# Optimization experiments

Hardware: AMD Instinct MI355X
Metric: run time of the kernel (lower is better)

Reference implementation:

```python
import jax, jax.numpy as jnp
import numpy as np

HIDDEN = 256


def setup_inputs() -> dict:
    key = jax.random.key(0)
    ks = jax.random.split(key, 6)
    b, c_len, q_len, h = 32, 1024, 128, HIDDEN
    # Xavier-uniform bounds for the learned weights
    lim_vec = float(np.sqrt(6.0 / (h + 1)))      # (h, 1) weights
    lim_cq = float(np.sqrt(6.0 / (1 + h)))       # (1, 1, h) weight
    return {
        "context": jax.random.normal(ks[0], (b, c_len, h), dtype=jnp.float32),
        "query": jax.random.normal(ks[1], (b, q_len, h), dtype=jnp.float32),
        "c_mask": jnp.zeros((b, c_len), dtype=bool),
        "q_mask": jnp.zeros((b, q_len), dtype=bool),
        "c_weight": jax.random.uniform(ks[2], (h, 1), jnp.float32, -lim_vec, lim_vec),
        "q_weight": jax.random.uniform(ks[3], (h, 1), jnp.float32, -lim_vec, lim_vec),
        "cq_weight": jax.random.uniform(ks[4], (1, 1, h), jnp.float32, -lim_cq, lim_cq),
        "bias": jnp.zeros((1,), dtype=jnp.float32),
    }


def reference(context, query, c_mask, q_mask, c_weight, q_weight, cq_weight, bias):
    # Trilinear similarity: S[b,i,j] = c_i.w_c + q_j.w_q + (c_i * w_cq).q_j + bias
    s0 = context @ c_weight                                  # (b, c, 1)
    s1 = jnp.swapaxes(query @ q_weight, 1, 2)                # (b, 1, q)
    s2 = jnp.einsum('bch,bqh->bcq', context * cq_weight, query)
    S = s0 + s1 + s2 + bias                                  # (b, c, q)

    S_bar = jax.nn.softmax(S, axis=1)       # softmax over context axis
    S_bar_bar = jax.nn.softmax(S, axis=2)   # softmax over query axis

    A = jnp.einsum('bcq,bqh->bch', S, query)  # note: raw S, as in source
    B = jnp.einsum('bcq,bkq,bkh->bch', S_bar, S_bar_bar, context)

    return jnp.concatenate([context, A, context * A, context * B], axis=2)
```

## Files before the change

kernel.cpp:

```cpp
#include <hip/hip_runtime.h>
#include <cstdint>
#include <cstddef>

#define BATCH 32
#define CLEN  1024
#define QLEN  128
#define HID   256

typedef __attribute__((ext_vector_type(8))) short bf16x8;
typedef __attribute__((ext_vector_type(4))) float f32x4;

#define MFMA(a, b, c) __builtin_amdgcn_mfma_f32_16x16x32_bf16((a), (b), (c), 0, 0, 0)

__device__ __forceinline__ ushort f2b(float f) {
    union { float f; uint u; } v; v.f = f;
    uint r = (v.u + 0x7fffu + ((v.u >> 16) & 1u)) >> 16;
    return (ushort)r;
}
__device__ __forceinline__ float b2f(ushort u) {
    union { uint u; float f; } v; v.u = ((uint)u) << 16;
    return v.f;
}

__global__ __launch_bounds__(256) void prep_kernel(
    const float* __restrict__ context, const float* __restrict__ query,
    const float* __restrict__ cw, const float* __restrict__ qw,
    const float* __restrict__ cqw,
    ushort* __restrict__ ctxB, ushort* __restrict__ ctxT,
    ushort* __restrict__ qmB, ushort* __restrict__ qT,
    float* __restrict__ cdot, float* __restrict__ qdot)
{
    __shared__ ushort lds[64][258];
    int bid = blockIdx.x;
    int t = threadIdx.x;
    int r = t >> 2, qd = t & 3;
    if (bid < 512) {
        int b = bid >> 4, c0 = (bid & 15) * 64;
        const float* src = context + ((size_t)(b * CLEN + c0 + r)) * HID;
        ushort* cbr = ctxB + ((size_t)(b * CLEN + c0 + r)) * HID;
        float dot = 0.f;
        #pragma unroll
        for (int j = 0; j < 16; j++) {
            int h = j * 16 + qd * 4;
            float4 v = *reinterpret_cast<const float4*>(src + h);
            float4 w = *reinterpret_cast<const float4*>(cw + h);
            dot += v.x * w.x + v.y * w.y + v.z * w.z + v.w * w.w;
            uint p0 = (uint)f2b(v.x) | ((uint)f2b(v.y) << 16);
            uint p1 = (uint)f2b(v.z) | ((uint)f2b(v.w) << 16);
            *reinterpret_cast<uint*>(&lds[r][h])     = p0;
            *reinterpret_cast<uint*>(&lds[r][h + 2]) = p1;
            uint2 pk; pk.x = p0; pk.y = p1;
            *reinterpret_cast<uint2*>(cbr + h) = pk;
        }
        dot += __shfl_xor(dot, 1);
        dot += __shfl_xor(dot, 2);
        if (qd == 0) cdot[b * CLEN + c0 + r] = dot;
        __syncthreads();
        ushort* dst = ctxT + ((size_t)(b * HID + t)) * CLEN + c0;
        #pragma unroll
        for (int j = 0; j < 8; j++) {
            uint4 w;
            w.x = (uint)lds[j*8+0][t] | ((uint)lds[j*8+1][t] << 16);
            w.y = (uint)lds[j*8+2][t] | ((uint)lds[j*8+3][t] << 16);
            w.z = (uint)lds[j*8+4][t] | ((uint)lds[j*8+5][t] << 16);
            w.w = (uint)lds[j*8+6][t] | ((uint)lds[j*8+7][t] << 16);
            *reinterpret_cast<uint4*>(dst + j * 8) = w;
        }
    } else {
        int bb = bid - 512;
        int b = bb >> 1, q0 = (bb & 1) * 64;
        const float* src = query + ((size_t)(b * QLEN + q0 + r)) * HID;
        ushort* qmr = qmB + ((size_t)(b * QLEN + q0 + r)) * HID;
        float dot = 0.f;
        #pragma unroll
        for (int j = 0; j < 16; j++) {
            int h = j * 16 + qd * 4;
            float4 v   = *reinterpret_cast<const float4*>(src + h);
            float4 w   = *reinterpret_cast<const float4*>(qw + h);
            float4 wc4 = *reinterpret_cast<const float4*>(cqw + h);
            dot += v.x * w.x + v.y * w.y + v.z * w.z + v.w * w.w;
            uint p0 = (uint)f2b(v.x) | ((uint)f2b(v.y) << 16);
            uint p1 = (uint)f2b(v.z) | ((uint)f2b(v.w) << 16);
            *reinterpret_cast<uint*>(&lds[r][h])     = p0;
            *reinterpret_cast<uint*>(&lds[r][h + 2]) = p1;
            uint2 mc;
            mc.x = (uint)f2b(v.x * wc4.x) | ((uint)f2b(v.y * wc4.y) << 16);
            mc.y = (uint)f2b(v.z * wc4.z) | ((uint)f2b(v.w * wc4.w) << 16);
            *reinterpret_cast<uint2*>(qmr + h) = mc;
        }
        dot += __shfl_xor(dot, 1);
        dot += __shfl_xor(dot, 2);
        if (qd == 0) qdot[b * QLEN + q0 + r] = dot;
        __syncthreads();
        ushort* dst = qT + ((size_t)(b * HID + t)) * QLEN + q0;
        #pragma unroll
        for (int j = 0; j < 8; j++) {
            uint4 w;
            w.x = (uint)lds[j*8+0][t] | ((uint)lds[j*8+1][t] << 16);
            w.y = (uint)lds[j*8+2][t] | ((uint)lds[j*8+3][t] << 16);
            w.z = (uint)lds[j*8+4][t] | ((uint)lds[j*8+5][t] << 16);
            w.w = (uint)lds[j*8+6][t] | ((uint)lds[j*8+7][t] << 16);
            *reinterpret_cast<uint4*>(dst + j * 8) = w;
        }
    }
}

__global__ __launch_bounds__(256) void s_kernel(
    const ushort* __restrict__ ctxB, const ushort* __restrict__ qmB,
    const float* __restrict__ cdot, const float* __restrict__ qdot,
    const float* __restrict__ bias,
    ushort* __restrict__ S, ushort* __restrict__ P2T,
    float* __restrict__ psum)
{
    __shared__ float ldsS[64][132];
    __shared__ float ldsM[64], ldsR[64];
    __shared__ float ldsP[2][128];
    int ct = blockIdx.x, b = blockIdx.y;
    int c0 = ct * 64;
    int t = threadIdx.x;
    int w = t >> 6, L = t & 63, g = L >> 4, ln = L & 15;
    int wr = w >> 1, wc = w & 1;

    f32x4 acc[2][4];
    #pragma unroll
    for (int mi = 0; mi < 2; mi++)
        #pragma unroll
        for (int ni = 0; ni < 4; ni++) acc[mi][ni] = (f32x4){0.f, 0.f, 0.f, 0.f};

    const ushort* aBase = ctxB + ((size_t)(b * CLEN + c0 + wr * 32)) * HID;
    const ushort* qBb   = qmB + ((size_t)(b * QLEN + wc * 64)) * HID;

    #pragma unroll 2
    for (int kk = 0; kk < 8; kk++) {
        int k = kk * 32 + g * 8;
        bf16x8 a[2], bq[4];
        #pragma unroll
        for (int mi = 0; mi < 2; mi++)
            a[mi] = *reinterpret_cast<const bf16x8*>(aBase + (size_t)(mi * 16 + ln) * HID + k);
        #pragma unroll
        for (int ni = 0; ni < 4; ni++)
            bq[ni] = *reinterpret_cast<const bf16x8*>(qBb + (size_t)(ni * 16 + ln) * HID + k);
        #pragma unroll
        for (int mi = 0; mi < 2; mi++)
            #pragma unroll
            for (int ni = 0; ni < 4; ni++)
                acc[mi][ni] = MFMA(a[mi], bq[ni], acc[mi][ni]);
    }

    float bv = bias[0];
    float qdv[4];
    #pragma unroll
    for (int ni = 0; ni < 4; ni++) qdv[ni] = qdot[b * QLEN + wc * 64 + ni * 16 + ln];
    #pragma unroll
    for (int mi = 0; mi < 2; mi++)
        #pragma unroll
        for (int r = 0; r < 4; r++) {
            int row = wr * 32 + mi * 16 + g * 4 + r;
            float cd = cdot[b * CLEN + c0 + row] + bv;
            #pragma unroll
            for (int ni = 0; ni < 4; ni++)
                ldsS[row][wc * 64 + ni * 16 + ln] = acc[mi][ni][r] + cd + qdv[ni];
        }
    __syncthreads();
    {
        int row = t >> 2, qs = (t & 3) * 32;
        float4 vr[8];
        float mx = -1e30f;
        #pragma unroll
        for (int j = 0; j < 8; j++) {
            vr[j] = *reinterpret_cast<const float4*>(&ldsS[row][qs + j * 4]);
            mx = fmaxf(mx, fmaxf(fmaxf(vr[j].x, vr[j].y), fmaxf(vr[j].z, vr[j].w)));
        }
        mx = fmaxf(mx, __shfl_xor(mx, 1));
        mx = fmaxf(mx, __shfl_xor(mx, 2));
        float s = 0.f;
        #pragma unroll
        for (int j = 0; j < 8; j++)
            s += __expf(vr[j].x - mx) + __expf(vr[j].y - mx) +
                 __expf(vr[j].z - mx) + __expf(vr[j].w - mx);
        s += __shfl_xor(s, 1);
        s += __shfl_xor(s, 2);
        if ((t & 3) == 0) { ldsM[row] = mx; ldsR[row] = 1.0f / s; }
    }
    __syncthreads();
    {
        const size_t Sbase = ((size_t)b * CLEN + c0) * QLEN;
        #pragma unroll
        for (int i = 0; i < 8; i++) {
            int flat = t + 256 * i;
            int q4 = flat & 31, c = flat >> 5;
            float4 v = *reinterpret_cast<const float4*>(&ldsS[c][q4 * 4]);
            uint2 pk;
            pk.x = (uint)f2b(v.x) | ((uint)f2b(v.y) << 16);
            pk.y = (uint)f2b(v.z) | ((uint)f2b(v.w) << 16);
            *reinterpret_cast<uint2*>(&S[Sbase + (size_t)c * QLEN + q4 * 4]) = pk;
        }
    }
    {
        int q = t >> 1, half = t & 1;
        ushort* dst = P2T + ((size_t)b * QLEN + q) * CLEN + c0 + half * 32;
        #pragma unroll
        for (int jo = 0; jo < 4; jo++) {
            uint pk[4];
            #pragma unroll
            for (int l = 0; l < 4; l++) {
                int c0l = half * 32 + jo * 8 + l * 2;
                float p0 = __expf(ldsS[c0l][q]     - ldsM[c0l])     * ldsR[c0l];
                float p1 = __expf(ldsS[c0l + 1][q] - ldsM[c0l + 1]) * ldsR[c0l + 1];
                pk[l] = (uint)f2b(p0) | ((uint)f2b(p1) << 16);
            }
            uint4 wv; wv.x = pk[0]; wv.y = pk[1]; wv.z = pk[2]; wv.w = pk[3];
            *reinterpret_cast<uint4*>(dst + jo * 8) = wv;
        }
    }
    {
        int q = t & 127, hf = t >> 7;
        float s = 0.f;
        #pragma unroll
        for (int cc = 0; cc < 32; cc++)
            s += __expf(b2f(f2b(ldsS[hf * 32 + cc][q])));
        ldsP[hf][q] = s;
    }
    __syncthreads();
    if (t < 128)
        psum[((size_t)b * 16 + ct) * QLEN + t] = ldsP[0][t] + ldsP[1][t];
}

__global__ __launch_bounds__(256) void t_kernel(
    const ushort* __restrict__ ctxT, const ushort* __restrict__ P2T,
    float* __restrict__ Tpart)
{
    int x = blockIdx.x, b = blockIdx.y;
    int h0 = (x >> 1) * 64, ks = x & 1;
    int t = threadIdx.x;
    int w = t >> 6, L = t & 63, g = L >> 4, ln = L & 15;
    int wr = w >> 1, wc = w & 1;

    f32x4 acc[2][4];
    #pragma unroll
    for (int mi = 0; mi < 2; mi++)
        #pragma unroll
        for (int ni = 0; ni < 4; ni++) acc[mi][ni] = (f32x4){0.f, 0.f, 0.f, 0.f};

    const ushort* aB = ctxT + ((size_t)(b * HID + h0 + wr * 32)) * CLEN + ks * 512;
    const ushort* bB = P2T + ((size_t)(b * QLEN + wc * 64)) * CLEN + ks * 512;

    #pragma unroll 2
    for (int kk = 0; kk < 16; kk++) {
        int k = kk * 32 + g * 8;
        bf16x8 a[2], bq[4];
        #pragma unroll
        for (int mi = 0; mi < 2; mi++)
            a[mi] = *reinterpret_cast<const bf16x8*>(aB + (size_t)(mi * 16 + ln) * CLEN + k);
        #pragma unroll
        for (int ni = 0; ni < 4; ni++)
            bq[ni] = *reinterpret_cast<const bf16x8*>(bB + (size_t)(ni * 16 + ln) * CLEN + k);
        #pragma unroll
        for (int mi = 0; mi < 2; mi++)
            #pragma unroll
            for (int ni = 0; ni < 4; ni++)
                acc[mi][ni] = MFMA(a[mi], bq[ni], acc[mi][ni]);
    }
    float* dst = Tpart + (size_t)ks * (BATCH * HID * QLEN);
    #pragma unroll
    for (int mi = 0; mi < 2; mi++)
        #pragma unroll
        for (int ni = 0; ni < 4; ni++)
            #pragma unroll
            for (int r = 0; r < 4; r++) {
                int h = h0 + wr * 32 + mi * 16 + g * 4 + r;
                int q = wc * 64 + ni * 16 + ln;
                dst[((size_t)b * HID + h) * QLEN + q] = acc[mi][ni][r];
            }
}

__global__ __launch_bounds__(256) void cs_kernel(
    const float* __restrict__ psum, const float* __restrict__ Tpart,
    ushort* __restrict__ Tt)
{
    __shared__ float SR[128];
    int hc = blockIdx.x, b = blockIdx.y;
    int t = threadIdx.x;
    if (t < 128) {
        float s = 0.f;
        #pragma unroll
        for (int j = 0; j < 16; j++)
            s += psum[((size_t)b * 16 + j) * QLEN + t];
        SR[t] = 1.0f / s;
    }
    __syncthreads();
    int h = hc * 32 + (t >> 3), qs = (t & 7) * 16;
    const float* p0 = Tpart + ((size_t)b * HID + h) * QLEN + qs;
    const float* p1 = p0 + (size_t)BATCH * HID * QLEN;
    uint pk[8];
    #pragma unroll
    for (int seg = 0; seg < 4; seg++) {
        float4 xa = *reinterpret_cast<const float4*>(p0 + seg * 4);
        float4 xb = *reinterpret_cast<const float4*>(p1 + seg * 4);
        float r0 = (xa.x + xb.x) * SR[qs + seg * 4 + 0];
        float r1 = (xa.y + xb.y) * SR[qs + seg * 4 + 1];
        float r2 = (xa.z + xb.z) * SR[qs + seg * 4 + 2];
        float r3 = (xa.w + xb.w) * SR[qs + seg * 4 + 3];
        pk[seg * 2 + 0] = (uint)f2b(r0) | ((uint)f2b(r1) << 16);
        pk[seg * 2 + 1] = (uint)f2b(r2) | ((uint)f2b(r3) << 16);
    }
    ushort* dst = Tt + ((size_t)b * HID + h) * QLEN + qs;
    uint4 w0; w0.x = pk[0]; w0.y = pk[1]; w0.z = pk[2]; w0.w = pk[3];
    uint4 w1; w1.x = pk[4]; w1.y = pk[5]; w1.z = pk[6]; w1.w = pk[7];
    *reinterpret_cast<uint4*>(dst)     = w0;
    *reinterpret_cast<uint4*>(dst + 8) = w1;
}

__global__ __launch_bounds__(256) void ab_out_kernel(
    const ushort* __restrict__ S, const ushort* __restrict__ qT,
    const ushort* __restrict__ Tt, const ushort* __restrict__ ctxB,
    float* __restrict__ out)
{
    __shared__ float ldsA[64][68];
    __shared__ float ldsB[64][68];
    int x = blockIdx.x, b = blockIdx.y;
    int c0 = (x & 15) * 64, h0 = (x >> 4) * 128;
    int t = threadIdx.x;
    int wv = t >> 6, L = t & 63, g = L >> 4, ln = L & 15;

    f32x4 accA[4][2], accB[4][2];
    #pragma unroll
    for (int mi = 0; mi < 4; mi++)
        #pragma unroll
        for (int ni = 0; ni < 2; ni++) {
            accA[mi][ni] = (f32x4){0.f, 0.f, 0.f, 0.f};
            accB[mi][ni] = (f32x4){0.f, 0.f, 0.f, 0.f};
        }

    const ushort* Srow = S + ((size_t)(b * CLEN + c0)) * QLEN;
    const ushort* qTb  = qT + ((size_t)(b * HID + h0 + wv * 32)) * QLEN;
    const ushort* TtB  = Tt + ((size_t)(b * HID + h0 + wv * 32)) * QLEN;

    #pragma unroll
    for (int kk = 0; kk < 4; kk++) {
        int k = kk * 32 + g * 8;
        bf16x8 sa[4], pa[4], bq[2], bt[2];
        #pragma unroll
        for (int mi = 0; mi < 4; mi++) {
            sa[mi] = *reinterpret_cast<const bf16x8*>(Srow + (size_t)(mi * 16 + ln) * QLEN + k);
            bf16x8 pv;
            #pragma unroll
            for (int i = 0; i < 8; i++)
                pv[i] = (short)f2b(__expf(b2f((ushort)sa[mi][i])));
            pa[mi] = pv;
        }
        #pragma unroll
        for (int ni = 0; ni < 2; ni++) {
            bq[ni] = *reinterpret_cast<const bf16x8*>(qTb + (size_t)(ni * 16 + ln) * QLEN + k);
            bt[ni] = *reinterpret_cast<const bf16x8*>(TtB + (size_t)(ni * 16 + ln) * QLEN + k);
        }
        #pragma unroll
        for (int mi = 0; mi < 4; mi++)
            #pragma unroll
            for (int ni = 0; ni < 2; ni++) {
                accA[mi][ni] = MFMA(sa[mi], bq[ni], accA[mi][ni]);
                accB[mi][ni] = MFMA(pa[mi], bt[ni], accB[mi][ni]);
            }
    }

    #pragma unroll
    for (int hh = 0; hh < 2; hh++) {
        if ((wv >> 1) == hh) {
            int hc = wv & 1;
            #pragma unroll
            for (int mi = 0; mi < 4; mi++)
                #pragma unroll
                for (int ni = 0; ni < 2; ni++)
                    #pragma unroll
                    for (int r = 0; r < 4; r++) {
                        ldsA[mi * 16 + g * 4 + r][hc * 32 + ni * 16 + ln] = accA[mi][ni][r];
                        ldsB[mi * 16 + g * 4 + r][hc * 32 + ni * 16 + ln] = accB[mi][ni][r];
                    }
        }
        __syncthreads();
        #pragma unroll
        for (int i = 0; i < 2; i++) {
            int flat = t + 256 * i;
            int h8 = flat & 7, c = flat >> 3;
            bf16x8 cb = *reinterpret_cast<const bf16x8*>(
                ctxB + ((size_t)(b * CLEN + c0 + c)) * HID + h0 + hh * 64 + h8 * 8);
            float cf[8];
            #pragma unroll
            for (int j = 0; j < 8; j++) cf[j] = b2f((ushort)cb[j]);
            float4 a0 = *reinterpret_cast<const float4*>(&ldsA[c][h8 * 8]);
            float4 a1 = *reinterpret_cast<const float4*>(&ldsA[c][h8 * 8 + 4]);
            float4 b0 = *reinterpret_cast<const float4*>(&ldsB[c][h8 * 8]);
            float4 b1 = *reinterpret_cast<const float4*>(&ldsB[c][h8 * 8 + 4]);
            size_t o = ((size_t)(b * CLEN + c0 + c)) * 1024 + h0 + hh * 64 + h8 * 8;
            *reinterpret_cast<float4*>(&out[o])     = make_float4(cf[0], cf[1], cf[2], cf[3]);
            *reinterpret_cast<float4*>(&out[o + 4]) = make_float4(cf[4], cf[5], cf[6], cf[7]);
            *reinterpret_cast<float4*>(&out[o + 256]) = a0;
            *reinterpret_cast<float4*>(&out[o + 260]) = a1;
            *reinterpret_cast<float4*>(&out[o + 512]) =
                make_float4(cf[0] * a0.x, cf[1] * a0.y, cf[2] * a0.z, cf[3] * a0.w);
            *reinterpret_cast<float4*>(&out[o + 516]) =
                make_float4(cf[4] * a1.x, cf[5] * a1.y, cf[6] * a1.z, cf[7] * a1.w);
            *reinterpret_cast<float4*>(&out[o + 768]) =
                make_float4(cf[0] * b0.x, cf[1] * b0.y, cf[2] * b0.z, cf[3] * b0.w);
            *reinterpret_cast<float4*>(&out[o + 772]) =
                make_float4(cf[4] * b1.x, cf[5] * b1.y, cf[6] * b1.z, cf[7] * b1.w);
        }
        __syncthreads();
    }
}

extern "C" void kernel_launch(void* const* d_in, const int* in_sizes, int n_in,
                              void* d_out, int out_size, void* d_ws, size_t ws_size,
                              hipStream_t stream)
{
    (void)in_sizes; (void)n_in; (void)out_size; (void)ws_size;
    const float* context   = (const float*)d_in[0];
    const float* query     = (const float*)d_in[1];
    const float* c_weight  = (const float*)d_in[4];
    const float* q_weight  = (const float*)d_in[5];
    const float* cq_weight = (const float*)d_in[6];
    const float* bias      = (const float*)d_in[7];
    float* out = (float*)d_out;
    char* wsb  = (char*)d_ws;

    ushort* ctxB = (ushort*)(wsb);
    ushort* ctxT = (ushort*)(wsb + 16777216);
    ushort* qmB  = (ushort*)(wsb + 33554432);
    ushort* qT   = (ushort*)(wsb + 35651584);
    ushort* S    = (ushort*)(wsb + 37748736);
    ushort* P2T  = (ushort*)(wsb + 46137344);
    ushort* Tt   = (ushort*)(wsb + 54525952);
    float*  Tpart = (float*)(wsb + 56623104);
    float*  cdot  = (float*)(wsb + 65011712);
    float*  qdot  = cdot + 32768;
    float*  psum  = qdot + 4096;

    prep_kernel<<<576, 256, 0, stream>>>(context, query, c_weight, q_weight,
                                         cq_weight, ctxB, ctxT, qmB, qT,
                                         cdot, qdot);
    s_kernel<<<dim3(16, 32), 256, 0, stream>>>(ctxB, qmB, cdot, qdot, bias,
                                               S, P2T, psum);
    t_kernel<<<dim3(8, 32), 256, 0, stream>>>(ctxT, P2T, Tpart);
    cs_kernel<<<dim3(8, 32), 256, 0, stream>>>(psum, Tpart, Tt);
    ab_out_kernel<<<dim3(32, 32), 256, 0, stream>>>(S, qT, Tt, ctxB, out);
}
```

Before: 99.82 us.

## Fuse split-K reduction and softmax scaling into output kernel; use nontemporal loads/stores

Removes the separate cs_kernel by having ab_out_kernel sum the two Tpart split-K partials, scale by the reciprocal column sums and convert to bf16 on the fly when building its MFMA B operands. This saves one launch and the Tt round trip through memory. In exchange, each of the 32 c-tile blocks now re-reads the fp32 partials, which is twice the bytes and redundant across blocks. It also switches the input loads in prep_kernel and the large output writes to nontemporal, to reduce cache pollution.

```diff
diff --git a/kernel.cpp b/kernel.cpp
--- a/kernel.cpp
+++ b/kernel.cpp
@@ -42,7 +42,8 @@
         #pragma unroll
         for (int j = 0; j < 16; j++) {
             int h = j * 16 + qd * 4;
-            float4 v = *reinterpret_cast<const float4*>(src + h);
+            f32x4 v = __builtin_nontemporal_load(
+                reinterpret_cast<const f32x4*>(src + h));
             float4 w = *reinterpret_cast<const float4*>(cw + h);
             dot += v.x * w.x + v.y * w.y + v.z * w.z + v.w * w.w;
             uint p0 = (uint)f2b(v.x) | ((uint)f2b(v.y) << 16);
@@ -75,7 +76,8 @@
         #pragma unroll
         for (int j = 0; j < 16; j++) {
             int h = j * 16 + qd * 4;
-            float4 v   = *reinterpret_cast<const float4*>(src + h);
+            f32x4 v = __builtin_nontemporal_load(
+                reinterpret_cast<const f32x4*>(src + h));
             float4 w   = *reinterpret_cast<const float4*>(qw + h);
             float4 wc4 = *reinterpret_cast<const float4*>(cqw + h);
             dot += v.x * w.x + v.y * w.y + v.z * w.z + v.w * w.w;
@@ -274,48 +276,12 @@
             }
 }
 
-__global__ __launch_bounds__(256) void cs_kernel(
-    const float* __restrict__ psum, const float* __restrict__ Tpart,
-    ushort* __restrict__ Tt)
+__global__ __launch_bounds__(256) void ab_out_kernel(
+    const ushort* __restrict__ S, const ushort* __restrict__ qT,
+    const float* __restrict__ Tpart, const float* __restrict__ psum,
+    const ushort* __restrict__ ctxB, float* __restrict__ out)
 {
     __shared__ float SR[128];
-    int hc = blockIdx.x, b = blockIdx.y;
-    int t = threadIdx.x;
-    if (t < 128) {
-        float s = 0.f;
-        #pragma unroll
-        for (int j = 0; j < 16; j++)
-            s += psum[((size_t)b * 16 + j) * QLEN + t];
-        SR[t] = 1.0f / s;
-    }
-    __syncthreads();
-    int h = hc * 32 + (t >> 3), qs = (t & 7) * 16;
-    const float* p0 = Tpart + ((size_t)b * HID + h) * QLEN + qs;
-    const float* p1 = p0 + (size_t)BATCH * HID * QLEN;
-    uint pk[8];
-    #pragma unroll
-    for (int seg = 0; seg < 4; seg++) {
-        float4 xa = *reinterpret_cast<const float4*>(p0 + seg * 4);
-        float4 xb = *reinterpret_cast<const float4*>(p1 + seg * 4);
-        float r0 = (xa.x + xb.x) * SR[qs + seg * 4 + 0];
-        float r1 = (xa.y + xb.y) * SR[qs + seg * 4 + 1];
-        float r2 = (xa.z + xb.z) * SR[qs + seg * 4 + 2];
-        float r3 = (xa.w + xb.w) * SR[qs + seg * 4 + 3];
-        pk[seg * 2 + 0] = (uint)f2b(r0) | ((uint)f2b(r1) << 16);
-        pk[seg * 2 + 1] = (uint)f2b(r2) | ((uint)f2b(r3) << 16);
-    }
-    ushort* dst = Tt + ((size_t)b * HID + h) * QLEN + qs;
-    uint4 w0; w0.x = pk[0]; w0.y = pk[1]; w0.z = pk[2]; w0.w = pk[3];
-    uint4 w1; w1.x = pk[4]; w1.y = pk[5]; w1.z = pk[6]; w1.w = pk[7];
-    *reinterpret_cast<uint4*>(dst)     = w0;
-    *reinterpret_cast<uint4*>(dst + 8) = w1;
-}
-
-__global__ __launch_bounds__(256) void ab_out_kernel(
-    const ushort* __restrict__ S, const ushort* __restrict__ qT,
-    const ushort* __restrict__ Tt, const ushort* __restrict__ ctxB,
-    float* __restrict__ out)
-{
     __shared__ float ldsA[64][68];
     __shared__ float ldsB[64][68];
     int x = blockIdx.x, b = blockIdx.y;
@@ -323,6 +289,15 @@
     int t = threadIdx.x;
     int wv = t >> 6, L = t & 63, g = L >> 4, ln = L & 15;
 
+    if (t < 128) {
+        float s = 0.f;
+        #pragma unroll
+        for (int j = 0; j < 16; j++)
+            s += psum[((size_t)b * 16 + j) * QLEN + t];
+        SR[t] = 1.0f / s;
+    }
+    __syncthreads();
+
     f32x4 accA[4][2], accB[4][2];
     #pragma unroll
     for (int mi = 0; mi < 4; mi++)
@@ -334,11 +309,19 @@
 
     const ushort* Srow = S + ((size_t)(b * CLEN + c0)) * QLEN;
     const ushort* qTb  = qT + ((size_t)(b * HID + h0 + wv * 32)) * QLEN;
-    const ushort* TtB  = Tt + ((size_t)(b * HID + h0 + wv * 32)) * QLEN;
+    const float* Tp0 = Tpart + ((size_t)(b * HID + h0 + wv * 32)) * QLEN;
+    const float* Tp1 = Tp0 + (size_t)BATCH * HID * QLEN;
 
     #pragma unroll
     for (int kk = 0; kk < 4; kk++) {
         int k = kk * 32 + g * 8;
+        float srv[8];
+        {
+            float4 s0 = *reinterpret_cast<const float4*>(&SR[k]);
+            float4 s1 = *reinterpret_cast<const float4*>(&SR[k + 4]);
+            srv[0]=s0.x; srv[1]=s0.y; srv[2]=s0.z; srv[3]=s0.w;
+            srv[4]=s1.x; srv[5]=s1.y; srv[6]=s1.z; srv[7]=s1.w;
+        }
         bf16x8 sa[4], pa[4], bq[2], bt[2];
         #pragma unroll
         for (int mi = 0; mi < 4; mi++) {
@@ -352,7 +335,22 @@
         #pragma unroll
         for (int ni = 0; ni < 2; ni++) {
             bq[ni] = *reinterpret_cast<const bf16x8*>(qTb + (size_t)(ni * 16 + ln) * QLEN + k);
-            bt[ni] = *reinterpret_cast<const bf16x8*>(TtB + (size_t)(ni * 16 + ln) * QLEN + k);
+            const float* p0 = Tp0 + (size_t)(ni * 16 + ln) * QLEN + k;
+            const float* p1 = Tp1 + (size_t)(ni * 16 + ln) * QLEN + k;
+            float4 x0 = *reinterpret_cast<const float4*>(p0);
+            float4 x1 = *reinterpret_cast<const float4*>(p0 + 4);
+            float4 y0 = *reinterpret_cast<const float4*>(p1);
+            float4 y1 = *reinterpret_cast<const float4*>(p1 + 4);
+            bf16x8 tv;
+            tv[0] = (short)f2b((x0.x + y0.x) * srv[0]);
+            tv[1] = (short)f2b((x0.y + y0.y) * srv[1]);
+            tv[2] = (short)f2b((x0.z + y0.z) * srv[2]);
+            tv[3] = (short)f2b((x0.w + y0.w) * srv[3]);
+            tv[4] = (short)f2b((x1.x + y1.x) * srv[4]);
+            tv[5] = (short)f2b((x1.y + y1.y) * srv[5]);
+            tv[6] = (short)f2b((x1.z + y1.z) * srv[6]);
+            tv[7] = (short)f2b((x1.w + y1.w) * srv[7]);
+            bt[ni] = tv;
         }
         #pragma unroll
         for (int mi = 0; mi < 4; mi++)
@@ -387,23 +385,21 @@
             float cf[8];
             #pragma unroll
             for (int j = 0; j < 8; j++) cf[j] = b2f((ushort)cb[j]);
-            float4 a0 = *reinterpret_cast<const float4*>(&ldsA[c][h8 * 8]);
-            float4 a1 = *reinterpret_cast<const float4*>(&ldsA[c][h8 * 8 + 4]);
-            float4 b0 = *reinterpret_cast<const float4*>(&ldsB[c][h8 * 8]);
-            float4 b1 = *reinterpret_cast<const float4*>(&ldsB[c][h8 * 8 + 4]);
+            f32x4 a0 = *reinterpret_cast<const f32x4*>(&ldsA[c][h8 * 8]);
+            f32x4 a1 = *reinterpret_cast<const f32x4*>(&ldsA[c][h8 * 8 + 4]);
+            f32x4 b0 = *reinterpret_cast<const f32x4*>(&ldsB[c][h8 * 8]);
+            f32x4 b1 = *reinterpret_cast<const f32x4*>(&ldsB[c][h8 * 8 + 4]);
             size_t o = ((size_t)(b * CLEN + c0 + c)) * 1024 + h0 + hh * 64 + h8 * 8;
-            *reinterpret_cast<float4*>(&out[o])     = make_float4(cf[0], cf[1], cf[2], cf[3]);
-            *reinterpret_cast<float4*>(&out[o + 4]) = make_float4(cf[4], cf[5], cf[6], cf[7]);
-            *reinterpret_cast<float4*>(&out[o + 256]) = a0;
-            *reinterpret_cast<float4*>(&out[o + 260]) = a1;
-            *reinterpret_cast<float4*>(&out[o + 512]) =
-                make_float4(cf[0] * a0.x, cf[1] * a0.y, cf[2] * a0.z, cf[3] * a0.w);
-            *reinterpret_cast<float4*>(&out[o + 516]) =
-                make_float4(cf[4] * a1.x, cf[5] * a1.y, cf[6] * a1.z, cf[7] * a1.w);
-            *reinterpret_cast<float4*>(&out[o + 768]) =
-                make_float4(cf[0] * b0.x, cf[1] * b0.y, cf[2] * b0.z, cf[3] * b0.w);
-            *reinterpret_cast<float4*>(&out[o + 772]) =
-                make_float4(cf[4] * b1.x, cf[5] * b1.y, cf[6] * b1.z, cf[7] * b1.w);
+            f32x4 c0v = {cf[0], cf[1], cf[2], cf[3]};
+            f32x4 c1v = {cf[4], cf[5], cf[6], cf[7]};
+            __builtin_nontemporal_store(c0v, reinterpret_cast<f32x4*>(&out[o]));
+            __builtin_nontemporal_store(c1v, reinterpret_cast<f32x4*>(&out[o + 4]));
+            __builtin_nontemporal_store(a0, reinterpret_cast<f32x4*>(&out[o + 256]));
+            __builtin_nontemporal_store(a1, reinterpret_cast<f32x4*>(&out[o + 260]));
+            __builtin_nontemporal_store(c0v * a0, reinterpret_cast<f32x4*>(&out[o + 512]));
+            __builtin_nontemporal_store(c1v * a1, reinterpret_cast<f32x4*>(&out[o + 516]));
+            __builtin_nontemporal_store(c0v * b0, reinterpret_cast<f32x4*>(&out[o + 768]));
+            __builtin_nontemporal_store(c1v * b1, reinterpret_cast<f32x4*>(&out[o + 772]));
         }
         __syncthreads();
     }
@@ -429,7 +425,6 @@
     ushort* qT   = (ushort*)(wsb + 35651584);
     ushort* S    = (ushort*)(wsb + 37748736);
     ushort* P2T  = (ushort*)(wsb + 46137344);
-    ushort* Tt   = (ushort*)(wsb + 54525952);
     float*  Tpart = (float*)(wsb + 56623104);
     float*  cdot  = (float*)(wsb + 65011712);
     float*  qdot  = cdot + 32768;
@@ -441,6 +436,5 @@
     s_kernel<<<dim3(16, 32), 256, 0, stream>>>(ctxB, qmB, cdot, qdot, bias,
                                                S, P2T, psum);
     t_kernel<<<dim3(8, 32), 256, 0, stream>>>(ctxT, P2T, Tpart);
-    cs_kernel<<<dim3(8, 32), 256, 0, stream>>>(psum, Tpart, Tt);
-    ab_out_kernel<<<dim3(32, 32), 256, 0, stream>>>(S, qT, Tt, ctxB, out);
-}
+    ab_out_kernel<<<dim3(32, 32), 256, 0, stream>>>(S, qT, Tpart, psum, ctxB, out);
+}
```

Measured after the change: 138.1 us. +38.4%, slower.

## Fuse T GEMM with column-sum normalization, dropping split-K partial buffer

Applied to the files above, without the earlier changes.

Merges t_kernel and cs_kernel. The GEMM now runs over the full 1024-long context dimension instead of two split-K halves, then scales each result by the reciprocal column sum and writes bf16 Tt directly. This removes a kernel launch and the fp32 Tpart write and readback. In exchange the grid halves to 128 blocks with twice the loop length, which lowers parallelism. The epilogue stores are scattered 2-byte writes.

```diff
diff --git a/kernel.cpp b/kernel.cpp
--- a/kernel.cpp
+++ b/kernel.cpp
@@ -228,58 +228,11 @@
 
 __global__ __launch_bounds__(256) void t_kernel(
     const ushort* __restrict__ ctxT, const ushort* __restrict__ P2T,
-    float* __restrict__ Tpart)
-{
-    int x = blockIdx.x, b = blockIdx.y;
-    int h0 = (x >> 1) * 64, ks = x & 1;
-    int t = threadIdx.x;
-    int w = t >> 6, L = t & 63, g = L >> 4, ln = L & 15;
-    int wr = w >> 1, wc = w & 1;
-
-    f32x4 acc[2][4];
-    #pragma unroll
-    for (int mi = 0; mi < 2; mi++)
-        #pragma unroll
-        for (int ni = 0; ni < 4; ni++) acc[mi][ni] = (f32x4){0.f, 0.f, 0.f, 0.f};
-
-    const ushort* aB = ctxT + ((size_t)(b * HID + h0 + wr * 32)) * CLEN + ks * 512;
-    const ushort* bB = P2T + ((size_t)(b * QLEN + wc * 64)) * CLEN + ks * 512;
-
-    #pragma unroll 2
-    for (int kk = 0; kk < 16; kk++) {
-        int k = kk * 32 + g * 8;
-        bf16x8 a[2], bq[4];
-        #pragma unroll
-        for (int mi = 0; mi < 2; mi++)
-            a[mi] = *reinterpret_cast<const bf16x8*>(aB + (size_t)(mi * 16 + ln) * CLEN + k);
-        #pragma unroll
-        for (int ni = 0; ni < 4; ni++)
-            bq[ni] = *reinterpret_cast<const bf16x8*>(bB + (size_t)(ni * 16 + ln) * CLEN + k);
-        #pragma unroll
-        for (int mi = 0; mi < 2; mi++)
-            #pragma unroll
-            for (int ni = 0; ni < 4; ni++)
-                acc[mi][ni] = MFMA(a[mi], bq[ni], acc[mi][ni]);
-    }
-    float* dst = Tpart + (size_t)ks * (BATCH * HID * QLEN);
-    #pragma unroll
-    for (int mi = 0; mi < 2; mi++)
-        #pragma unroll
-        for (int ni = 0; ni < 4; ni++)
-            #pragma unroll
-            for (int r = 0; r < 4; r++) {
-                int h = h0 + wr * 32 + mi * 16 + g * 4 + r;
-                int q = wc * 64 + ni * 16 + ln;
-                dst[((size_t)b * HID + h) * QLEN + q] = acc[mi][ni][r];
-            }
-}
-
-__global__ __launch_bounds__(256) void cs_kernel(
-    const float* __restrict__ psum, const float* __restrict__ Tpart,
-    ushort* __restrict__ Tt)
+    const float* __restrict__ psum, ushort* __restrict__ Tt)
 {
     __shared__ float SR[128];
-    int hc = blockIdx.x, b = blockIdx.y;
+    int x = blockIdx.x, b = blockIdx.y;
+    int h0 = x * 64;
     int t = threadIdx.x;
     if (t < 128) {
         float s = 0.f;
@@ -289,26 +242,46 @@
         SR[t] = 1.0f / s;
     }
     __syncthreads();
-    int h = hc * 32 + (t >> 3), qs = (t & 7) * 16;
-    const float* p0 = Tpart + ((size_t)b * HID + h) * QLEN + qs;
-    const float* p1 = p0 + (size_t)BATCH * HID * QLEN;
-    uint pk[8];
-    #pragma unroll
-    for (int seg = 0; seg < 4; seg++) {
-        float4 xa = *reinterpret_cast<const float4*>(p0 + seg * 4);
-        float4 xb = *reinterpret_cast<const float4*>(p1 + seg * 4);
-        float r0 = (xa.x + xb.x) * SR[qs + seg * 4 + 0];
-        float r1 = (xa.y + xb.y) * SR[qs + seg * 4 + 1];
-        float r2 = (xa.z + xb.z) * SR[qs + seg * 4 + 2];
-        float r3 = (xa.w + xb.w) * SR[qs + seg * 4 + 3];
-        pk[seg * 2 + 0] = (uint)f2b(r0) | ((uint)f2b(r1) << 16);
-        pk[seg * 2 + 1] = (uint)f2b(r2) | ((uint)f2b(r3) << 16);
-    }
-    ushort* dst = Tt + ((size_t)b * HID + h) * QLEN + qs;
-    uint4 w0; w0.x = pk[0]; w0.y = pk[1]; w0.z = pk[2]; w0.w = pk[3];
-    uint4 w1; w1.x = pk[4]; w1.y = pk[5]; w1.z = pk[6]; w1.w = pk[7];
-    *reinterpret_cast<uint4*>(dst)     = w0;
-    *reinterpret_cast<uint4*>(dst + 8) = w1;
+    int w = t >> 6, L = t & 63, g = L >> 4, ln = L & 15;
+    int wr = w >> 1, wc = w & 1;
+
+    f32x4 acc[2][4];
+    #pragma unroll
+    for (int mi = 0; mi < 2; mi++)
+        #pragma unroll
+        for (int ni = 0; ni < 4; ni++) acc[mi][ni] = (f32x4){0.f, 0.f, 0.f, 0.f};
+
+    const ushort* aB = ctxT + ((size_t)(b * HID + h0 + wr * 32)) * CLEN;
+    const ushort* bB = P2T + ((size_t)(b * QLEN + wc * 64)) * CLEN;
+
+    #pragma unroll 2
+    for (int kk = 0; kk < 32; kk++) {
+        int k = kk * 32 + g * 8;
+        bf16x8 a[2], bq[4];
+        #pragma unroll
+        for (int mi = 0; mi < 2; mi++)
+            a[mi] = *reinterpret_cast<const bf16x8*>(aB + (size_t)(mi * 16 + ln) * CLEN + k);
+        #pragma unroll
+        for (int ni = 0; ni < 4; ni++)
+            bq[ni] = *reinterpret_cast<const bf16x8*>(bB + (size_t)(ni * 16 + ln) * CLEN + k);
+        #pragma unroll
+        for (int mi = 0; mi < 2; mi++)
+            #pragma unroll
+            for (int ni = 0; ni < 4; ni++)
+                acc[mi][ni] = MFMA(a[mi], bq[ni], acc[mi][ni]);
+    }
+    #pragma unroll
+    for (int mi = 0; mi < 2; mi++)
+        #pragma unroll
+        for (int ni = 0; ni < 4; ni++) {
+            int q = wc * 64 + ni * 16 + ln;
+            float cr = SR[q];
+            #pragma unroll
+            for (int r = 0; r < 4; r++) {
+                int h = h0 + wr * 32 + mi * 16 + g * 4 + r;
+                Tt[((size_t)b * HID + h) * QLEN + q] = f2b(acc[mi][ni][r] * cr);
+            }
+        }
 }
 
 __global__ __launch_bounds__(256) void ab_out_kernel(
@@ -430,17 +403,15 @@
     ushort* S    = (ushort*)(wsb + 37748736);
     ushort* P2T  = (ushort*)(wsb + 46137344);
     ushort* Tt   = (ushort*)(wsb + 54525952);
-    float*  Tpart = (float*)(wsb + 56623104);
-    float*  cdot  = (float*)(wsb + 65011712);
-    float*  qdot  = cdot + 32768;
-    float*  psum  = qdot + 4096;
+    float*  cdot = (float*)(wsb + 56623104);
+    float*  qdot = cdot + 32768;
+    float*  psum = qdot + 4096;
 
     prep_kernel<<<576, 256, 0, stream>>>(context, query, c_weight, q_weight,
                                          cq_weight, ctxB, ctxT, qmB, qT,
                                          cdot, qdot);
     s_kernel<<<dim3(16, 32), 256, 0, stream>>>(ctxB, qmB, cdot, qdot, bias,
                                                S, P2T, psum);
-    t_kernel<<<dim3(8, 32), 256, 0, stream>>>(ctxT, P2T, Tpart);
-    cs_kernel<<<dim3(8, 32), 256, 0, stream>>>(psum, Tpart, Tt);
+    t_kernel<<<dim3(4, 32), 256, 0, stream>>>(ctxT, P2T, psum, Tt);
     ab_out_kernel<<<dim3(32, 32), 256, 0, stream>>>(S, qT, Tt, ctxB, out);
 }
```

Measured after the change: 106.3 us. 6.5% more time.
